# Optimization experiments

Hardware: AMD Instinct MI355X
Metric: run time of the kernel (lower is better)

The kernel has to match this reference:

```python
import jax, jax.numpy as jnp
import numpy as np

B, QS, KS, E, H = 2, 2048, 2048, 2048, 16
D = E // H  # head_dim = 128
EPS = 1e-6


def setup_inputs() -> dict:
    key = jax.random.key(0)
    ks = jax.random.split(key, 11)
    scale_in = 1.0 / np.sqrt(E)  # lecun_normal fan_in = E
    scale_out = 1.0 / np.sqrt(E)  # fan_in for out proj = H*D = E
    return {
        "q": jax.random.normal(ks[0], (B, QS, E), jnp.float32),
        "kv": jax.random.normal(ks[1], (B, KS, E), jnp.float32),
        "q_pos": jax.random.normal(ks[2], (B, QS, E), jnp.float32),
        "kv_pos": jax.random.normal(ks[3], (B, KS, E), jnp.float32),
        "mask": jax.random.bernoulli(ks[4], 0.5, (B, QS, KS)),
        "wq": jax.random.normal(ks[5], (E, H, D), jnp.float32) * scale_in,
        "wk": jax.random.normal(ks[6], (E, H, D), jnp.float32) * scale_in,
        "wv": jax.random.normal(ks[7], (E, H, D), jnp.float32) * scale_in,
        "q_ln_scale": jnp.ones((D,), jnp.float32),
        "k_ln_scale": jnp.ones((D,), jnp.float32),
        "wo": jax.random.normal(ks[8], (H, D, E), jnp.float32) * scale_out,
    }


def _layernorm_no_bias(x, scale):
    # flax LayerNorm over last axis, use_bias=False, epsilon=1e-6
    mu = jnp.mean(x, axis=-1, keepdims=True)
    var = jnp.mean(jnp.square(x - mu), axis=-1, keepdims=True)
    return (x - mu) * jax.lax.rsqrt(var + EPS) * scale


def reference(q, kv, q_pos, kv_pos, mask, wq, wk, wv, q_ln_scale, k_ln_scale, wo):
    dtype = q.dtype
    qi = q + q_pos          # [b, qs, e]
    ki = kv + kv_pos        # [b, ks, e]
    vi = kv
    # QKV projections (DenseGeneral, no bias) -> [b, s, h, d]
    qh = jnp.einsum('bqe,ehd->bqhd', qi, wq)
    kh = jnp.einsum('bke,ehd->bkhd', ki, wk)
    vh = jnp.einsum('bke,ehd->bkhd', vi, wv)
    # normalize_qk: LayerNorm (no bias) on query/key over head_dim
    qh = _layernorm_no_bias(qh, q_ln_scale)
    kh = _layernorm_no_bias(kh, k_ln_scale)
    # scaled dot-product with float32 logits
    qh = qh / jnp.sqrt(jnp.asarray(D, dtype))
    logits = jnp.einsum('bqhd,bkhd->bhqk', qh, kh,
                        preferred_element_type=jnp.float32)
    big_neg = jnp.finfo(jnp.float32).min
    logits = jnp.where(mask[:, None, :, :], logits, big_neg)
    attn = jax.nn.softmax(logits, axis=-1).astype(dtype)  # [b,h,q,k]
    out = jnp.einsum('bhqk,bkhd->bqhd', attn, vh)
    # output projection (DenseGeneral over (h,d), no bias)
    return jnp.einsum('bqhd,hde->bqe', out, wo)
```

## Files before the change

kernel.cpp:

```cpp
#include <hip/hip_runtime.h>
#include <hip/hip_bf16.h>


typedef __attribute__((ext_vector_type(8))) __bf16 bf16x8;
typedef __attribute__((ext_vector_type(4))) float f32x4;
typedef __attribute__((ext_vector_type(8))) unsigned short ushort8;
typedef __attribute__((ext_vector_type(4))) unsigned short ushort4v;
typedef __attribute__((ext_vector_type(4))) unsigned uint4v;
typedef __attribute__((ext_vector_type(4))) float float4v;

#define MFMA16(a, b, c) __builtin_amdgcn_mfma_f32_16x16x32_bf16((a), (b), (c), 0, 0, 0)

__device__ __forceinline__ unsigned short f2bf(float f) {
  unsigned u = __builtin_bit_cast(unsigned, f);
  u += 0x7fffu + ((u >> 16) & 1u);
  return (unsigned short)(u >> 16);
}

__device__ __forceinline__ unsigned pkbf(float lo, float hi) {
  unsigned d;
  asm("v_cvt_pk_bf16_f32 %0, %1, %2" : "=v"(d) : "v"(lo), "v"(hi));
  return d;
}

__device__ __forceinline__ float max3f(float a, float b, float c) {
  float d;
  asm("v_max3_f32 %0, %1, %2, %3" : "=v"(d) : "v"(a), "v"(b), "v"(c));
  return d;
}

__device__ __forceinline__ float exp2a(float x) {
  float d;
  asm("v_exp_f32 %0, %1" : "=v"(d) : "v"(x));
  return d;
}

__device__ __forceinline__ void gload_lds16(const void* g, void* l) {
  __builtin_amdgcn_global_load_lds(
      (const __attribute__((address_space(1))) void*)g,
      (__attribute__((address_space(3))) void*)l, 16, 0, 0);
}

__global__ __launch_bounds__(256) void k_cvt(const float4v* __restrict__ x,
                                             const float4v* __restrict__ y,
                                             ushort4v* __restrict__ o, int n4) {
  int i = blockIdx.x * 256 + threadIdx.x;
  if (i >= n4) return;
  float4v a = x[i];
  if (y) { float4v b = y[i]; a = a + b; }
  ushort4v r;
  r[0] = f2bf(a[0]); r[1] = f2bf(a[1]); r[2] = f2bf(a[2]); r[3] = f2bf(a[3]);
  o[i] = r;
}

__global__ __launch_bounds__(256) void k_cvt2(const float4v* __restrict__ x,
                                              const float4v* __restrict__ y,
                                              ushort4v* __restrict__ oa,
                                              ushort4v* __restrict__ ob, int n4) {
  int i = blockIdx.x * 256 + threadIdx.x;
  if (i >= n4) return;
  float4v a = x[i];
  float4v s = a + y[i];
  ushort4v ra, rb;
  ra[0] = f2bf(s[0]); ra[1] = f2bf(s[1]); ra[2] = f2bf(s[2]); ra[3] = f2bf(s[3]);
  rb[0] = f2bf(a[0]); rb[1] = f2bf(a[1]); rb[2] = f2bf(a[2]); rb[3] = f2bf(a[3]);
  oa[i] = ra; ob[i] = rb;
}

__global__ __launch_bounds__(256) void k_tr(const float* __restrict__ s0, const float* __restrict__ s1,
                                            const float* __restrict__ s2, const float* __restrict__ s3,
                                            unsigned short* __restrict__ d0, unsigned short* __restrict__ d1,
                                            unsigned short* __restrict__ d2, unsigned short* __restrict__ d3) {
  __shared__ float t[32][33];
  const float* S; unsigned short* D;
  switch (blockIdx.z) {
    case 0: S = s0; D = d0; break;
    case 1: S = s1; D = d1; break;
    case 2: S = s2; D = d2; break;
    default: S = s3; D = d3; break;
  }
  int x = threadIdx.x & 31, y = threadIdx.x >> 5;
  int r0 = blockIdx.y * 32, c0 = blockIdx.x * 32;
#pragma unroll
  for (int i = 0; i < 4; ++i) t[y + 8 * i][x] = S[(size_t)(r0 + y + 8 * i) * 2048 + c0 + x];
  __syncthreads();
#pragma unroll
  for (int i = 0; i < 4; ++i)
    D[(size_t)(c0 + y + 8 * i) * 2048 + r0 + x] = f2bf(t[x][y + 8 * i]);
}

__global__ __launch_bounds__(256) void k_mask(const int* __restrict__ m,
                                              unsigned long long* __restrict__ out) {
  int i = blockIdx.x * 256 + threadIdx.x;
  unsigned long long b = __ballot(m[i] != 0);
  if ((threadIdx.x & 63) == 0) out[i >> 6] = b;
}

__global__ __launch_bounds__(256) void k_trv(const unsigned short* __restrict__ Vh,
                                             unsigned short* __restrict__ Vt) {
  __shared__ unsigned short t[64][72];
  int bh = blockIdx.z;
  int s0 = blockIdx.x * 64, d0 = blockIdx.y * 64;
  size_t base = (size_t)bh * 2048 * 128;
  int row = threadIdx.x >> 2, c16 = (threadIdx.x & 3) * 16;
  {
    const unsigned short* src = Vh + base + (size_t)(s0 + row) * 128 + d0 + c16;
    ushort8 a0 = *(const ushort8*)src;
    ushort8 a1 = *(const ushort8*)(src + 8);
#pragma unroll
    for (int e = 0; e < 8; ++e) {
      t[c16 + e][row] = a0[e];
      t[c16 + 8 + e][row] = a1[e];
    }
  }
  __syncthreads();
  {
    unsigned short* dst = Vt + base + (size_t)(d0 + row) * 2048 + s0 + c16;
    *(ushort8*)dst = *(const ushort8*)&t[row][c16];
    *(ushort8*)(dst + 8) = *(const ushort8*)&t[row][c16 + 8];
  }
}

template <int MODE>
__global__ __launch_bounds__(256) void k_gemm(const unsigned short* __restrict__ A,
                                              const unsigned short* __restrict__ Bt,
                                              void* __restrict__ Cv,
                                              const float* __restrict__ lnsc) {
  constexpr int K = 2048;
  __shared__ __attribute__((aligned(16))) unsigned short sA[128 * 64];
  __shared__ __attribute__((aligned(16))) unsigned short sB[128 * 64];
  __shared__ float sSum[2][128];
  __shared__ float sSq[2][128];
  int tid = threadIdx.x;
  int lane = tid & 63, w = tid >> 6;
  int wr = w >> 1, wc = w & 1;
  int r15 = lane & 15, blk = lane >> 4;
  int n0 = blockIdx.x * 128, m0 = blockIdx.y * 128;
  const unsigned short* Abase = A + (size_t)m0 * K;
  const unsigned short* Bbase = Bt + (size_t)n0 * K;
  f32x4 acc[4][4] = {};

  for (int kt = 0; kt < K; kt += 64) {
#pragma unroll
    for (int i = 0; i < 4; ++i) {
      int c = i * 256 + tid;
      int row = c >> 3, cc = c & 7;
      gload_lds16(Abase + (size_t)row * K + kt + ((cc ^ (row & 7)) * 8), &sA[c * 8]);
    }
#pragma unroll
    for (int i = 0; i < 4; ++i) {
      int c = i * 256 + tid;
      int row = c >> 3, cc = c & 7;
      gload_lds16(Bbase + (size_t)row * K + kt + ((cc ^ (row & 7)) * 8), &sB[c * 8]);
    }
    __syncthreads();
#pragma unroll
    for (int kk = 0; kk < 2; ++kk) {
      bf16x8 av[4], bv[4];
#pragma unroll
      for (int i = 0; i < 4; ++i) {
        int row = wr * 64 + i * 16 + r15;
        av[i] = *(const bf16x8*)&sA[row * 64 + (((kk * 4 + blk) ^ (row & 7)) * 8)];
      }
#pragma unroll
      for (int j = 0; j < 4; ++j) {
        int row = wc * 64 + j * 16 + r15;
        bv[j] = *(const bf16x8*)&sB[row * 64 + (((kk * 4 + blk) ^ (row & 7)) * 8)];
      }
#pragma unroll
      for (int i = 0; i < 4; ++i)
#pragma unroll
        for (int j = 0; j < 4; ++j) acc[i][j] = MFMA16(av[i], bv[j], acc[i][j]);
    }
    __syncthreads();
  }

  if constexpr (MODE == 3) {
    float* C = (float*)Cv;
#pragma unroll
    for (int i = 0; i < 4; ++i)
#pragma unroll
      for (int r = 0; r < 4; ++r)
#pragma unroll
        for (int j = 0; j < 4; ++j) {
          int rowl = wr * 64 + i * 16 + blk * 4 + r;
          int coll = wc * 64 + j * 16 + r15;
          C[(size_t)(m0 + rowl) * 2048 + n0 + coll] = acc[i][j][r];
        }
    return;
  } else {
    if constexpr (MODE == 1 || MODE == 2) {
#pragma unroll
      for (int i = 0; i < 4; ++i)
#pragma unroll
        for (int r = 0; r < 4; ++r) {
          float sm = 0.f, sq = 0.f;
#pragma unroll
          for (int j = 0; j < 4; ++j) { float v = acc[i][j][r]; sm += v; sq += v * v; }
          sm += __shfl_xor(sm, 1); sq += __shfl_xor(sq, 1);
          sm += __shfl_xor(sm, 2); sq += __shfl_xor(sq, 2);
          sm += __shfl_xor(sm, 4); sq += __shfl_xor(sq, 4);
          sm += __shfl_xor(sm, 8); sq += __shfl_xor(sq, 8);
          if (r15 == 0) {
            int rowl = wr * 64 + i * 16 + blk * 4 + r;
            sSum[wc][rowl] = sm; sSq[wc][rowl] = sq;
          }
        }
      __syncthreads();
    }
    unsigned short* Hout = (unsigned short*)Cv;
    int h = blockIdx.x;
#pragma unroll
    for (int i = 0; i < 4; ++i)
#pragma unroll
      for (int r = 0; r < 4; ++r) {
        int rowl = wr * 64 + i * 16 + blk * 4 + r;
        float mean = 0.f, rstd = 1.f;
        if constexpr (MODE == 1 || MODE == 2) {
          float sm = sSum[0][rowl] + sSum[1][rowl];
          float sq = sSq[0][rowl] + sSq[1][rowl];
          mean = sm * 0.0078125f;
          float var = sq * 0.0078125f - mean * mean;
          rstd = rsqrtf(var + 1e-6f);
        }
        int rowg = m0 + rowl;
        int b = rowg >> 11, s = rowg & 2047;
        unsigned short* orow = Hout + (((size_t)b * 16 + h) * 2048 + s) * 128;
#pragma unroll
        for (int j = 0; j < 4; ++j) {
          int d = wc * 64 + j * 16 + r15;
          float v = acc[i][j][r];
          if constexpr (MODE == 1)
            v = (v - mean) * rstd * lnsc[d] * (0.08838834764831845f * 1.4426950408889634f);
          if constexpr (MODE == 2) v = (v - mean) * rstd * lnsc[d];
          orow[d] = f2bf(v);
        }
      }
  }
}

__global__ __launch_bounds__(256, 4) void k_attn(const unsigned short* __restrict__ Qh,
                                                 const unsigned short* __restrict__ Kh,
                                                 const unsigned short* __restrict__ Vt,
                                                 const unsigned* __restrict__ maskb,
                                                 unsigned short* __restrict__ O) {
  __shared__ __attribute__((aligned(16))) char smem[64 * 132 * 4];
  unsigned short* sK = (unsigned short*)smem;
  unsigned short* sV = (unsigned short*)(smem + 16384);
  float* sO = (float*)smem;

  int tid = threadIdx.x, w = tid >> 6;
  int lane = tid & 63;
  int r15 = lane & 15, blk = lane >> 4;
  int bh = blockIdx.y, b = bh >> 4, h = bh & 15;
  int qb = blockIdx.x * 64;
  size_t base = (size_t)bh * (2048 * 128);
  int qrow = qb + w * 16 + r15;

  bf16x8 qf[4];
  {
    const unsigned short* qp = Qh + base + (size_t)qrow * 128 + blk * 8;
#pragma unroll
    for (int kk = 0; kk < 4; ++kk) qf[kk] = *(const bf16x8*)(qp + kk * 32);
  }
  const unsigned* mrow = maskb + ((size_t)b * 2048 + qrow) * 64;

  const unsigned short* kp[4];
  const unsigned short* vp[4];
  unsigned short* kl[4];
  unsigned short* vl[4];
#pragma unroll
  for (int i = 0; i < 4; ++i) {
    int c = i * 256 + tid;
    int krow = c >> 4, kcc = c & 15;
    int key = 32 * (krow >> 5) + 8 * ((krow >> 2) & 3) + 4 * ((krow >> 4) & 1) + (krow & 3);
    kp[i] = Kh + base + (size_t)key * 128 + ((kcc ^ (krow & 7)) * 8);
    kl[i] = &sK[c * 8];
    int d = c >> 3, c8 = c & 7;
    vp[i] = Vt + base + (size_t)d * 2048 + ((c8 ^ (d & 7)) * 8);
    vl[i] = &sV[c * 8];
  }

  f32x4 o[8] = {};
  float m = -1e30f, lsum = 0.f;

  for (int kc = 0; kc < 2048; kc += 64) {
#pragma unroll
    for (int i = 0; i < 4; ++i) { gload_lds16(kp[i], kl[i]); kp[i] += 64 * 128; }
#pragma unroll
    for (int i = 0; i < 4; ++i) { gload_lds16(vp[i], vl[i]); vp[i] += 64; }
    __syncthreads();

    f32x4 st[4] = {};
#pragma unroll
    for (int kk = 0; kk < 4; ++kk) {
      int cc = (4 * kk + blk) ^ (r15 & 7);
#pragma unroll
      for (int s = 0; s < 4; ++s) {
        bf16x8 kf = *(const bf16x8*)&sK[(16 * s + r15) * 128 + cc * 8];
        st[s] = MFMA16(kf, qf[kk], st[s]);
      }
    }

    unsigned mws0 = mrow[kc >> 5] >> (blk * 8);
    unsigned mws1 = mrow[(kc >> 5) + 1] >> (blk * 8);
    float pvv[16];
#pragma unroll
    for (int t = 0; t < 16; ++t) {
      int s = t >> 2, r = t & 3;
      unsigned mws = (s & 2) ? mws1 : mws0;
      int bit = 4 * (s & 1) + r;
      pvv[t] = ((mws >> bit) & 1u) ? st[s][r] : -1e30f;
    }
    float c0 = max3f(pvv[0], pvv[1], pvv[2]);
    float c1 = max3f(pvv[3], pvv[4], pvv[5]);
    float c2 = max3f(pvv[6], pvv[7], pvv[8]);
    float c3 = max3f(pvv[9], pvv[10], pvv[11]);
    float c4 = max3f(pvv[12], pvv[13], pvv[14]);
    float cmax = fmaxf(max3f(c0, c1, c2), max3f(c3, c4, pvv[15]));
    cmax = fmaxf(cmax, __shfl_xor(cmax, 16));
    cmax = fmaxf(cmax, __shfl_xor(cmax, 32));

    if (!__all(cmax - m <= 11.5f)) {
      float mnew = fmaxf(m, cmax);
      float fac = exp2a(m - mnew);
      lsum *= fac;
      float fr[4];
#pragma unroll
      for (int r = 0; r < 4; ++r) fr[r] = __shfl(fac, blk * 4 + r);
#pragma unroll
      for (int t8 = 0; t8 < 8; ++t8) {
        o[t8][0] *= fr[0]; o[t8][1] *= fr[1]; o[t8][2] *= fr[2]; o[t8][3] *= fr[3];
      }
      m = mnew;
    }

#pragma unroll
    for (int t = 0; t < 16; ++t) pvv[t] = exp2a(pvv[t] - m);
    float s0 = (pvv[0] + pvv[1]) + (pvv[2] + pvv[3]);
    float s1 = (pvv[4] + pvv[5]) + (pvv[6] + pvv[7]);
    float s2 = (pvv[8] + pvv[9]) + (pvv[10] + pvv[11]);
    float s3 = (pvv[12] + pvv[13]) + (pvv[14] + pvv[15]);
    lsum += (s0 + s1) + (s2 + s3);

    uint4v w0, w1;
#pragma unroll
    for (int j = 0; j < 4; ++j) {
      w0[j] = pkbf(pvv[2 * j], pvv[2 * j + 1]);
      w1[j] = pkbf(pvv[8 + 2 * j], pvv[9 + 2 * j]);
    }
    bf16x8 pf0 = __builtin_bit_cast(bf16x8, w0);
    bf16x8 pf1 = __builtin_bit_cast(bf16x8, w1);

#pragma unroll
    for (int t8 = 0; t8 < 8; ++t8) {
      int vr = t8 * 16 + r15;
      bf16x8 v0 = *(const bf16x8*)&sV[vr * 64 + ((blk ^ (r15 & 7)) * 8)];
      bf16x8 v1 = *(const bf16x8*)&sV[vr * 64 + (((4 + blk) ^ (r15 & 7)) * 8)];
      o[t8] = MFMA16(pf0, v0, o[t8]);
      o[t8] = MFMA16(pf1, v1, o[t8]);
    }
    __syncthreads();
  }

  lsum += __shfl_xor(lsum, 16);
  lsum += __shfl_xor(lsum, 32);
  float inv = 1.f / lsum;
  float ir[4];
#pragma unroll
  for (int r = 0; r < 4; ++r) ir[r] = __shfl(inv, blk * 4 + r);
#pragma unroll
  for (int t8 = 0; t8 < 8; ++t8)
#pragma unroll
    for (int r = 0; r < 4; ++r)
      sO[(w * 16 + blk * 4 + r) * 132 + t8 * 16 + r15] = o[t8][r] * ir[r];
  __syncthreads();
  {
    int row = tid >> 2, d0 = (tid & 3) * 32;
    unsigned short* op = O + (size_t)(b * 2048 + qb + row) * 2048 + h * 128 + d0;
#pragma unroll
    for (int g = 0; g < 4; ++g) {
      ushort8 pk;
#pragma unroll
      for (int e = 0; e < 8; ++e) pk[e] = f2bf(sO[row * 132 + d0 + g * 8 + e]);
      *(ushort8*)(op + g * 8) = pk;
    }
  }
}

extern "C" void kernel_launch(void* const* d_in, const int* in_sizes, int n_in,
                              void* d_out, int out_size, void* d_ws, size_t ws_size,
                              hipStream_t stream) {
  const float* q      = (const float*)d_in[0];
  const float* kv     = (const float*)d_in[1];
  const float* q_pos  = (const float*)d_in[2];
  const float* kv_pos = (const float*)d_in[3];
  const int*   mask   = (const int*)d_in[4];
  const float* wq     = (const float*)d_in[5];
  const float* wk     = (const float*)d_in[6];
  const float* wv     = (const float*)d_in[7];
  const float* qls    = (const float*)d_in[8];
  const float* kls    = (const float*)d_in[9];
  const float* wo     = (const float*)d_in[10];

  char* ws = (char*)d_ws;
  const size_t SZ_ACT = (size_t)4096 * 2048 * 2;
  const size_t SZ_W   = (size_t)2048 * 2048 * 2;
  unsigned short* a_q = (unsigned short*)(ws);
  unsigned short* a_k = (unsigned short*)(ws + SZ_ACT);
  unsigned short* a_v = (unsigned short*)(ws + 2 * SZ_ACT);
  unsigned short* Qh  = (unsigned short*)(ws + 3 * SZ_ACT);
  unsigned short* Kh  = (unsigned short*)(ws + 4 * SZ_ACT);
  unsigned short* Vh  = (unsigned short*)(ws + 5 * SZ_ACT);
  unsigned short* wqt = (unsigned short*)(ws + 6 * SZ_ACT);
  unsigned short* wkt = (unsigned short*)(ws + 6 * SZ_ACT + SZ_W);
  unsigned short* wvt = (unsigned short*)(ws + 6 * SZ_ACT + 2 * SZ_W);
  unsigned short* wot = (unsigned short*)(ws + 6 * SZ_ACT + 3 * SZ_W);
  unsigned*       mkb = (unsigned*)(ws + 6 * SZ_ACT + 4 * SZ_W);
  unsigned short* Ob  = a_q;
  unsigned short* Vtr = a_k;

  const size_t NEED = 6 * SZ_ACT + 4 * SZ_W + (size_t)2 * 2048 * 64 * 4;
  if (ws_size < NEED) return;

  k_cvt<<<8192, 256, 0, stream>>>((const float4v*)q, (const float4v*)q_pos, (ushort4v*)a_q, 2097152);
  k_cvt2<<<8192, 256, 0, stream>>>((const float4v*)kv, (const float4v*)kv_pos,
                                   (ushort4v*)a_k, (ushort4v*)a_v, 2097152);
  k_tr<<<dim3(64, 64, 4), 256, 0, stream>>>(wq, wk, wv, wo, wqt, wkt, wvt, wot);
  k_mask<<<32768, 256, 0, stream>>>(mask, (unsigned long long*)mkb);

  k_gemm<1><<<dim3(16, 32), 256, 0, stream>>>(a_q, wqt, Qh, qls);
  k_gemm<2><<<dim3(16, 32), 256, 0, stream>>>(a_k, wkt, Kh, kls);
  k_gemm<0><<<dim3(16, 32), 256, 0, stream>>>(a_v, wvt, Vh, nullptr);

  k_trv<<<dim3(32, 2, 32), 256, 0, stream>>>(Vh, Vtr);

  k_attn<<<dim3(32, 32), 256, 0, stream>>>(Qh, Kh, Vtr, mkb, Ob);

  k_gemm<3><<<dim3(16, 32), 256, 0, stream>>>(Ob, wot, d_out, nullptr);
}
```

Measured before the change: 362.0 us.

## Double-buffer K/V tiles and process two query row groups per wave in attention

The attention kernel now handles 128 query rows per block, with each wave computing two 16-row groups. That reuses each K/V fragment read from LDS for twice the MFMA work. K/V tiles are double-buffered in 64KB of shared memory, so the next tile's global-to-LDS loads overlap compute on the current one, and one barrier per iteration is dropped. The costs are higher register pressure (launch bounds lowered to 2 blocks per SM), half as many blocks (512), and a two-pass output epilogue.

```diff
diff --git a/kernel.cpp b/kernel.cpp
--- a/kernel.cpp
+++ b/kernel.cpp
@@ -239,151 +239,209 @@
   }
 }
 
-__global__ __launch_bounds__(256, 4) void k_attn(const unsigned short* __restrict__ Qh,
+__device__ __forceinline__ void softmax_grp(const f32x4 (&st)[4], unsigned mw0, unsigned mw1,
+                                            int blk, float& mv, float& ls,
+                                            f32x4 (&o)[8], bf16x8& plo, bf16x8& phi) {
+  unsigned mws0 = mw0 >> (blk * 8);
+  unsigned mws1 = mw1 >> (blk * 8);
+  float pvv[16];
+#pragma unroll
+  for (int t = 0; t < 16; ++t) {
+    int s = t >> 2, r = t & 3;
+    unsigned mws = (s & 2) ? mws1 : mws0;
+    int bit = 4 * (s & 1) + r;
+    pvv[t] = ((mws >> bit) & 1u) ? st[s][r] : -1e30f;
+  }
+  float c0 = max3f(pvv[0], pvv[1], pvv[2]);
+  float c1 = max3f(pvv[3], pvv[4], pvv[5]);
+  float c2 = max3f(pvv[6], pvv[7], pvv[8]);
+  float c3 = max3f(pvv[9], pvv[10], pvv[11]);
+  float c4 = max3f(pvv[12], pvv[13], pvv[14]);
+  float cmax = fmaxf(max3f(c0, c1, c2), max3f(c3, c4, pvv[15]));
+  cmax = fmaxf(cmax, __shfl_xor(cmax, 16));
+  cmax = fmaxf(cmax, __shfl_xor(cmax, 32));
+  if (!__all(cmax - mv <= 11.5f)) {
+    float mnew = fmaxf(mv, cmax);
+    float fac = exp2a(mv - mnew);
+    ls *= fac;
+    float fr0 = __shfl(fac, blk * 4 + 0);
+    float fr1 = __shfl(fac, blk * 4 + 1);
+    float fr2 = __shfl(fac, blk * 4 + 2);
+    float fr3 = __shfl(fac, blk * 4 + 3);
+#pragma unroll
+    for (int t8 = 0; t8 < 8; ++t8) {
+      o[t8][0] *= fr0; o[t8][1] *= fr1; o[t8][2] *= fr2; o[t8][3] *= fr3;
+    }
+    mv = mnew;
+  }
+#pragma unroll
+  for (int t = 0; t < 16; ++t) pvv[t] = exp2a(pvv[t] - mv);
+  float s0 = (pvv[0] + pvv[1]) + (pvv[2] + pvv[3]);
+  float s1 = (pvv[4] + pvv[5]) + (pvv[6] + pvv[7]);
+  float s2 = (pvv[8] + pvv[9]) + (pvv[10] + pvv[11]);
+  float s3 = (pvv[12] + pvv[13]) + (pvv[14] + pvv[15]);
+  ls += (s0 + s1) + (s2 + s3);
+  uint4v w0, w1;
+#pragma unroll
+  for (int j = 0; j < 4; ++j) {
+    w0[j] = pkbf(pvv[2 * j], pvv[2 * j + 1]);
+    w1[j] = pkbf(pvv[8 + 2 * j], pvv[9 + 2 * j]);
+  }
+  plo = __builtin_bit_cast(bf16x8, w0);
+  phi = __builtin_bit_cast(bf16x8, w1);
+}
+
+__global__ __launch_bounds__(256, 2) void k_attn(const unsigned short* __restrict__ Qh,
                                                  const unsigned short* __restrict__ Kh,
                                                  const unsigned short* __restrict__ Vt,
                                                  const unsigned* __restrict__ maskb,
                                                  unsigned short* __restrict__ O) {
-  __shared__ __attribute__((aligned(16))) char smem[64 * 132 * 4];
-  unsigned short* sK = (unsigned short*)smem;
-  unsigned short* sV = (unsigned short*)(smem + 16384);
-  float* sO = (float*)smem;
-
+  __shared__ __attribute__((aligned(16))) char smem[65536];
   int tid = threadIdx.x, w = tid >> 6;
   int lane = tid & 63;
   int r15 = lane & 15, blk = lane >> 4;
   int bh = blockIdx.y, b = bh >> 4, h = bh & 15;
-  int qb = blockIdx.x * 64;
+  int qb = blockIdx.x * 128;
   size_t base = (size_t)bh * (2048 * 128);
-  int qrow = qb + w * 16 + r15;
-
-  bf16x8 qf[4];
-  {
-    const unsigned short* qp = Qh + base + (size_t)qrow * 128 + blk * 8;
-#pragma unroll
-    for (int kk = 0; kk < 4; ++kk) qf[kk] = *(const bf16x8*)(qp + kk * 32);
-  }
-  const unsigned* mrow = maskb + ((size_t)b * 2048 + qrow) * 64;
-
-  const unsigned short* kp[4];
-  const unsigned short* vp[4];
-  unsigned short* kl[4];
-  unsigned short* vl[4];
+  int qrow0 = qb + w * 32 + r15;
+  int qrow1 = qrow0 + 16;
+
+  bf16x8 qf0[4], qf1[4];
+  {
+    const unsigned short* qp0 = Qh + base + (size_t)qrow0 * 128 + blk * 8;
+    const unsigned short* qp1 = Qh + base + (size_t)qrow1 * 128 + blk * 8;
+#pragma unroll
+    for (int kk = 0; kk < 4; ++kk) {
+      qf0[kk] = *(const bf16x8*)(qp0 + kk * 32);
+      qf1[kk] = *(const bf16x8*)(qp1 + kk * 32);
+    }
+  }
+  const unsigned* mrow0 = maskb + ((size_t)b * 2048 + qrow0) * 64;
+  const unsigned* mrow1 = maskb + ((size_t)b * 2048 + qrow1) * 64;
+
+  const unsigned short* kgp[4];
+  const unsigned short* vgp[4];
 #pragma unroll
   for (int i = 0; i < 4; ++i) {
     int c = i * 256 + tid;
     int krow = c >> 4, kcc = c & 15;
     int key = 32 * (krow >> 5) + 8 * ((krow >> 2) & 3) + 4 * ((krow >> 4) & 1) + (krow & 3);
-    kp[i] = Kh + base + (size_t)key * 128 + ((kcc ^ (krow & 7)) * 8);
-    kl[i] = &sK[c * 8];
+    kgp[i] = Kh + base + (size_t)key * 128 + ((kcc ^ (krow & 7)) * 8);
     int d = c >> 3, c8 = c & 7;
-    vp[i] = Vt + base + (size_t)d * 2048 + ((c8 ^ (d & 7)) * 8);
-    vl[i] = &sV[c * 8];
-  }
-
-  f32x4 o[8] = {};
-  float m = -1e30f, lsum = 0.f;
-
+    vgp[i] = Vt + base + (size_t)d * 2048 + ((c8 ^ (d & 7)) * 8);
+  }
+
+  f32x4 o0[8] = {}, o1[8] = {};
+  float m0v = -1e30f, l0 = 0.f, m1v = -1e30f, l1 = 0.f;
+
+#pragma unroll
+  for (int i = 0; i < 4; ++i) {
+    int c = i * 256 + tid;
+    gload_lds16(kgp[i], (unsigned short*)smem + c * 8);
+    gload_lds16(vgp[i], (unsigned short*)(smem + 16384) + c * 8);
+  }
+  __syncthreads();
+
+  int cur = 0;
   for (int kc = 0; kc < 2048; kc += 64) {
-#pragma unroll
-    for (int i = 0; i < 4; ++i) { gload_lds16(kp[i], kl[i]); kp[i] += 64 * 128; }
-#pragma unroll
-    for (int i = 0; i < 4; ++i) { gload_lds16(vp[i], vl[i]); vp[i] += 64; }
-    __syncthreads();
-
-    f32x4 st[4] = {};
+    if (kc + 64 < 2048) {
+      char* nb = smem + ((cur ^ 1) << 15);
+#pragma unroll
+      for (int i = 0; i < 4; ++i) {
+        int c = i * 256 + tid;
+        gload_lds16(kgp[i] + (size_t)(kc + 64) * 128, (unsigned short*)nb + c * 8);
+        gload_lds16(vgp[i] + (kc + 64), (unsigned short*)(nb + 16384) + c * 8);
+      }
+    }
+    const unsigned short* sK = (const unsigned short*)(smem + (cur << 15));
+    const unsigned short* sV = (const unsigned short*)(smem + (cur << 15) + 16384);
+
+    f32x4 st0[4] = {}, st1[4] = {};
 #pragma unroll
     for (int kk = 0; kk < 4; ++kk) {
       int cc = (4 * kk + blk) ^ (r15 & 7);
 #pragma unroll
       for (int s = 0; s < 4; ++s) {
         bf16x8 kf = *(const bf16x8*)&sK[(16 * s + r15) * 128 + cc * 8];
-        st[s] = MFMA16(kf, qf[kk], st[s]);
+        st0[s] = MFMA16(kf, qf0[kk], st0[s]);
+        st1[s] = MFMA16(kf, qf1[kk], st1[s]);
       }
     }
 
-    unsigned mws0 = mrow[kc >> 5] >> (blk * 8);
-    unsigned mws1 = mrow[(kc >> 5) + 1] >> (blk * 8);
-    float pvv[16];
-#pragma unroll
-    for (int t = 0; t < 16; ++t) {
-      int s = t >> 2, r = t & 3;
-      unsigned mws = (s & 2) ? mws1 : mws0;
-      int bit = 4 * (s & 1) + r;
-      pvv[t] = ((mws >> bit) & 1u) ? st[s][r] : -1e30f;
-    }
-    float c0 = max3f(pvv[0], pvv[1], pvv[2]);
-    float c1 = max3f(pvv[3], pvv[4], pvv[5]);
-    float c2 = max3f(pvv[6], pvv[7], pvv[8]);
-    float c3 = max3f(pvv[9], pvv[10], pvv[11]);
-    float c4 = max3f(pvv[12], pvv[13], pvv[14]);
-    float cmax = fmaxf(max3f(c0, c1, c2), max3f(c3, c4, pvv[15]));
-    cmax = fmaxf(cmax, __shfl_xor(cmax, 16));
-    cmax = fmaxf(cmax, __shfl_xor(cmax, 32));
-
-    if (!__all(cmax - m <= 11.5f)) {
-      float mnew = fmaxf(m, cmax);
-      float fac = exp2a(m - mnew);
-      lsum *= fac;
-      float fr[4];
-#pragma unroll
-      for (int r = 0; r < 4; ++r) fr[r] = __shfl(fac, blk * 4 + r);
-#pragma unroll
-      for (int t8 = 0; t8 < 8; ++t8) {
-        o[t8][0] *= fr[0]; o[t8][1] *= fr[1]; o[t8][2] *= fr[2]; o[t8][3] *= fr[3];
-      }
-      m = mnew;
-    }
-
-#pragma unroll
-    for (int t = 0; t < 16; ++t) pvv[t] = exp2a(pvv[t] - m);
-    float s0 = (pvv[0] + pvv[1]) + (pvv[2] + pvv[3]);
-    float s1 = (pvv[4] + pvv[5]) + (pvv[6] + pvv[7]);
-    float s2 = (pvv[8] + pvv[9]) + (pvv[10] + pvv[11]);
-    float s3 = (pvv[12] + pvv[13]) + (pvv[14] + pvv[15]);
-    lsum += (s0 + s1) + (s2 + s3);
-
-    uint4v w0, w1;
-#pragma unroll
-    for (int j = 0; j < 4; ++j) {
-      w0[j] = pkbf(pvv[2 * j], pvv[2 * j + 1]);
-      w1[j] = pkbf(pvv[8 + 2 * j], pvv[9 + 2 * j]);
-    }
-    bf16x8 pf0 = __builtin_bit_cast(bf16x8, w0);
-    bf16x8 pf1 = __builtin_bit_cast(bf16x8, w1);
+    unsigned a0 = mrow0[kc >> 5], a1 = mrow0[(kc >> 5) + 1];
+    unsigned b0 = mrow1[kc >> 5], b1 = mrow1[(kc >> 5) + 1];
+    bf16x8 pf00, pf01, pf10, pf11;
+    softmax_grp(st0, a0, a1, blk, m0v, l0, o0, pf00, pf01);
+    softmax_grp(st1, b0, b1, blk, m1v, l1, o1, pf10, pf11);
 
 #pragma unroll
     for (int t8 = 0; t8 < 8; ++t8) {
       int vr = t8 * 16 + r15;
       bf16x8 v0 = *(const bf16x8*)&sV[vr * 64 + ((blk ^ (r15 & 7)) * 8)];
       bf16x8 v1 = *(const bf16x8*)&sV[vr * 64 + (((4 + blk) ^ (r15 & 7)) * 8)];
-      o[t8] = MFMA16(pf0, v0, o[t8]);
-      o[t8] = MFMA16(pf1, v1, o[t8]);
+      o0[t8] = MFMA16(pf00, v0, o0[t8]);
+      o0[t8] = MFMA16(pf01, v1, o0[t8]);
+      o1[t8] = MFMA16(pf10, v0, o1[t8]);
+      o1[t8] = MFMA16(pf11, v1, o1[t8]);
     }
     __syncthreads();
-  }
-
-  lsum += __shfl_xor(lsum, 16);
-  lsum += __shfl_xor(lsum, 32);
-  float inv = 1.f / lsum;
-  float ir[4];
-#pragma unroll
-  for (int r = 0; r < 4; ++r) ir[r] = __shfl(inv, blk * 4 + r);
-#pragma unroll
-  for (int t8 = 0; t8 < 8; ++t8)
-#pragma unroll
-    for (int r = 0; r < 4; ++r)
-      sO[(w * 16 + blk * 4 + r) * 132 + t8 * 16 + r15] = o[t8][r] * ir[r];
+    cur ^= 1;
+  }
+
+  float* sO = (float*)smem;
+  {
+    l0 += __shfl_xor(l0, 16); l0 += __shfl_xor(l0, 32);
+    float inv = 1.f / l0;
+    float ir0 = __shfl(inv, blk * 4 + 0), ir1 = __shfl(inv, blk * 4 + 1);
+    float ir2 = __shfl(inv, blk * 4 + 2), ir3 = __shfl(inv, blk * 4 + 3);
+#pragma unroll
+    for (int t8 = 0; t8 < 8; ++t8) {
+      int bi = (w * 16 + blk * 4) * 132 + t8 * 16 + r15;
+      sO[bi] = o0[t8][0] * ir0;
+      sO[bi + 132] = o0[t8][1] * ir1;
+      sO[bi + 264] = o0[t8][2] * ir2;
+      sO[bi + 396] = o0[t8][3] * ir3;
+    }
+  }
   __syncthreads();
   {
     int row = tid >> 2, d0 = (tid & 3) * 32;
-    unsigned short* op = O + (size_t)(b * 2048 + qb + row) * 2048 + h * 128 + d0;
-#pragma unroll
-    for (int g = 0; g < 4; ++g) {
+    int grow = qb + (row >> 4) * 32 + (row & 15);
+    unsigned short* op = O + (size_t)(b * 2048 + grow) * 2048 + h * 128 + d0;
+#pragma unroll
+    for (int g4 = 0; g4 < 4; ++g4) {
       ushort8 pk;
 #pragma unroll
-      for (int e = 0; e < 8; ++e) pk[e] = f2bf(sO[row * 132 + d0 + g * 8 + e]);
-      *(ushort8*)(op + g * 8) = pk;
+      for (int e = 0; e < 8; ++e) pk[e] = f2bf(sO[row * 132 + d0 + g4 * 8 + e]);
+      *(ushort8*)(op + g4 * 8) = pk;
+    }
+  }
+  __syncthreads();
+  {
+    l1 += __shfl_xor(l1, 16); l1 += __shfl_xor(l1, 32);
+    float inv = 1.f / l1;
+    float ir0 = __shfl(inv, blk * 4 + 0), ir1 = __shfl(inv, blk * 4 + 1);
+    float ir2 = __shfl(inv, blk * 4 + 2), ir3 = __shfl(inv, blk * 4 + 3);
+#pragma unroll
+    for (int t8 = 0; t8 < 8; ++t8) {
+      int bi = (w * 16 + blk * 4) * 132 + t8 * 16 + r15;
+      sO[bi] = o1[t8][0] * ir0;
+      sO[bi + 132] = o1[t8][1] * ir1;
+      sO[bi + 264] = o1[t8][2] * ir2;
+      sO[bi + 396] = o1[t8][3] * ir3;
+    }
+  }
+  __syncthreads();
+  {
+    int row = tid >> 2, d0 = (tid & 3) * 32;
+    int grow = qb + (row >> 4) * 32 + 16 + (row & 15);
+    unsigned short* op = O + (size_t)(b * 2048 + grow) * 2048 + h * 128 + d0;
+#pragma unroll
+    for (int g4 = 0; g4 < 4; ++g4) {
+      ushort8 pk;
+#pragma unroll
+      for (int e = 0; e < 8; ++e) pk[e] = f2bf(sO[row * 132 + d0 + g4 * 8 + e]);
+      *(ushort8*)(op + g4 * 8) = pk;
     }
   }
 }
@@ -435,7 +493,7 @@
 
   k_trv<<<dim3(32, 2, 32), 256, 0, stream>>>(Vh, Vtr);
 
-  k_attn<<<dim3(32, 32), 256, 0, stream>>>(Qh, Kh, Vtr, mkb, Ob);
+  k_attn<<<dim3(16, 32), 256, 0, stream>>>(Qh, Kh, Vtr, mkb, Ob);
 
   k_gemm<3><<<dim3(16, 32), 256, 0, stream>>>(Ob, wot, d_out, nullptr);
 }
```

Measured after the change: 353.1 us. -2.5%, faster.
